# Kernel optimization log

Hardware: AMD Instinct MI355X
Metric: run time of the kernel (lower is better)

Reference implementation:

```python
import jax, jax.numpy as jnp
import numpy as np

N_CLASS, EMB, NH = 32000, 128, 256
B, T = 2048, 256


def setup_inputs() -> dict:
    key = jax.random.key(0)
    ks = iter(jax.random.split(key, 40))
    d = {}
    d["X"] = jax.random.randint(next(ks), (B, T), 0, N_CLASS)
    d["C"] = jax.random.normal(next(ks), (N_CLASS, EMB), jnp.float32) * 0.02
    for g in "ifco":
        d[f"U_{g}1"] = jax.random.normal(next(ks), (EMB, NH), jnp.float32) / np.sqrt(EMB)
        d[f"V_{g}1"] = jax.random.normal(next(ks), (NH, NH), jnp.float32) / np.sqrt(NH)
        d[f"U_{g}2"] = jax.random.normal(next(ks), (NH, NH), jnp.float32) / np.sqrt(NH)
        d[f"V_{g}2"] = jax.random.normal(next(ks), (NH, NH), jnp.float32) / np.sqrt(NH)
        d[f"b_{g}1"] = jnp.ones((NH,), jnp.float32)
    d["W_out"] = jax.random.normal(next(ks), (NH, N_CLASS), jnp.float32) / np.sqrt(NH)
    d["b_out"] = jnp.ones((N_CLASS,), jnp.float32)
    return d


def reference(X, C,
              U_i1, V_i1, U_i2, V_i2, b_i1,
              U_f1, V_f1, U_f2, V_f2, b_f1,
              U_c1, V_c1, U_c2, V_c2, b_c1,
              U_o1, V_o1, U_o2, V_o2, b_o1,
              W_out, b_out):
    # Embed then move time to the leading axis: [T, B, EMB]
    xs = jnp.transpose(C[X], (1, 0, 2))
    Bsz = X.shape[0]
    dtype = C.dtype
    z = jnp.zeros((Bsz, NH), dtype)

    def step(carry, x):
        h1, c1, h2, c2 = carry
        # layer 1 LSTM cell
        f1 = jax.nn.sigmoid(x @ U_f1 + h1 @ V_f1 + b_f1)
        i1 = jax.nn.sigmoid(x @ U_i1 + h1 @ V_i1 + b_i1)
        g1 = jnp.tanh(x @ U_c1 + h1 @ V_c1 + b_c1)
        c1n = c1 * f1 + i1 * g1
        o1 = jax.nn.sigmoid(x @ U_o1 + h1 @ V_o1 + b_o1)
        h1n = o1 * jnp.tanh(c1n)
        # layer 2 LSTM cell (NOTE: original code reuses layer-1 biases here)
        f2 = jax.nn.sigmoid(h1n @ U_f2 + h2 @ V_f2 + b_f1)
        i2 = jax.nn.sigmoid(h1n @ U_i2 + h2 @ V_i2 + b_i1)
        g2 = jnp.tanh(h1n @ U_c2 + h2 @ V_c2 + b_c1)
        c2n = c2 * f2 + i2 * g2
        o2 = jax.nn.sigmoid(h1n @ U_o2 + h2 @ V_o2 + b_o1)
        h2n = o2 * jnp.tanh(c2n)
        return (h1n, c1n, h2n, c2n), None

    (h1, c1, h2, c2), _ = jax.lax.scan(step, (z, z, z, z), xs)
    return h2 @ W_out + b_out  # [B, N_CLASS]
```

## Files before the change

### kernel.cpp

```cpp
#include <hip/hip_runtime.h>
#include <hip/hip_bf16.h>

#define B_SZ   2048
#define T_SZ   256
#define EMB    128
#define NH     256
#define NCLASS 32000

typedef __bf16 bf16;
typedef __bf16 bf16x8 __attribute__((ext_vector_type(8)));
typedef __bf16 bf16x4 __attribute__((ext_vector_type(4)));
typedef float  f32x4  __attribute__((ext_vector_type(4)));

__device__ __forceinline__ float sigf(float x)      { return 1.0f / (1.0f + __expf(-x)); }
__device__ __forceinline__ float tanhfast(float x)  { return 2.0f / (1.0f + __expf(-2.0f * x)) - 1.0f; }

struct GatePtrs {
    const float* U1[4];
    const float* V1[4];
    const float* U2[4];
    const float* V2[4];
};

__global__ void prep_w1(GatePtrs gp, bf16* __restrict__ Wt1) {
    int gc = blockIdx.x;
    int k  = threadIdx.x;
    int g  = (gc >> 4) & 3;
    int nh = ((gc >> 6) << 4) | (gc & 15);
    float v = (k < EMB) ? gp.U1[g][k * NH + nh] : gp.V1[g][(k - EMB) * NH + nh];
    Wt1[gc * 384 + k] = (bf16)v;
}

__global__ void prep_w2(GatePtrs gp, bf16* __restrict__ Wt2) {
    int gc = blockIdx.x;
    int k  = threadIdx.x;
    int g  = (gc >> 4) & 3;
    int nh = ((gc >> 6) << 4) | (gc & 15);
    float v = (k < NH) ? gp.U2[g][k * NH + nh] : gp.V2[g][(k - NH) * NH + nh];
    Wt2[gc * 512 + k] = (bf16)v;
}

__global__ void prep_wo(const float* __restrict__ Wo, bf16* __restrict__ WoT) {
    __shared__ float tile[32][33];
    int n0 = blockIdx.x * 32;
    int k0 = blockIdx.y * 32;
    int tx = threadIdx.x & 31;
    int ty = threadIdx.x >> 5;
#pragma unroll
    for (int i = 0; i < 4; i++) {
        int k = k0 + ty + i * 8;
        tile[ty + i * 8][tx] = Wo[(size_t)k * NCLASS + n0 + tx];
    }
    __syncthreads();
#pragma unroll
    for (int i = 0; i < 4; i++) {
        int n = n0 + ty + i * 8;
        WoT[(size_t)n * NH + k0 + tx] = (bf16)tile[tx][ty + i * 8];
    }
}

__global__ void prep_xe(const int* __restrict__ X, const float* __restrict__ C,
                        bf16* __restrict__ Xe) {
    size_t id = (size_t)blockIdx.x * 256 + threadIdx.x;
    int c4 = (int)(id & 31) * 4;
    int b  = (int)(id >> 5) & (B_SZ - 1);
    int t  = (int)(id >> 16);
    int idx = X[b * T_SZ + t];
    float4 v = *(const float4*)(C + (size_t)idx * EMB + c4);
    bf16x4 hv;
    hv[0] = (bf16)v.x; hv[1] = (bf16)v.y; hv[2] = (bf16)v.z; hv[3] = (bf16)v.w;
    *(bf16x4*)(Xe + ((size_t)t * B_SZ + b) * EMB + c4) = hv;
}

template<int PRE>
__global__ __launch_bounds__(1024, 1) void lstm_kernel(
    const int* __restrict__ X, const float* __restrict__ C,
    const bf16* __restrict__ Wt1, const bf16* __restrict__ Wt2,
    const float* __restrict__ bi, const float* __restrict__ bf_,
    const float* __restrict__ bc, const float* __restrict__ bo,
    const bf16* __restrict__ Xe,
    bf16* __restrict__ h2out)
{
    __shared__ bf16 A1[2][32][392];
    __shared__ bf16 A2[2][32][520];

    const int tid  = threadIdx.x;
    const int lane = tid & 63;
    const int wv   = tid >> 6;
    const int cl   = lane & 15;
    const int quad = lane >> 4;
    const int gb   = blockIdx.x * 32;

    const float* bp[4] = { bi, bf_, bc, bo };
    float bias[4];
#pragma unroll
    for (int g = 0; g < 4; g++) bias[g] = bp[g][wv * 16 + cl];

    const bf16* w1p[4];
    const bf16* w2p[4];
#pragma unroll
    for (int g = 0; g < 4; g++) {
        int gc = wv * 64 + g * 16 + cl;
        w1p[g] = Wt1 + gc * 384 + quad * 8;
        w2p[g] = Wt2 + gc * 512 + quad * 8;
    }

    for (int i = tid; i < 8192; i += 1024) {
        int r = i >> 8, c = i & 255;
        A1[0][r][128 + c] = (bf16)0.0f;
        A2[0][r][256 + c] = (bf16)0.0f;
    }
    {
        int r  = tid >> 5;
        int cc = (tid & 31) * 4;
        if (PRE) {
            bf16x4 hv = *(const bf16x4*)(Xe + ((size_t)0 * B_SZ + gb + r) * EMB + cc);
            *(bf16x4*)&A1[0][r][cc] = hv;
        } else {
            int idx = X[(gb + r) * T_SZ + 0];
            float4 v = *(const float4*)(C + (size_t)idx * EMB + cc);
            bf16x4 hv;
            hv[0] = (bf16)v.x; hv[1] = (bf16)v.y; hv[2] = (bf16)v.z; hv[3] = (bf16)v.w;
            *(bf16x4*)&A1[0][r][cc] = hv;
        }
    }

    f32x4 c1s[2], c2s[2];
    const f32x4 zf = { 0.0f, 0.0f, 0.0f, 0.0f };
#pragma unroll
    for (int mt = 0; mt < 2; mt++) { c1s[mt] = zf; c2s[mt] = zf; }

    __syncthreads();

    for (int t = 0; t < T_SZ; t++) {
        const int p = t & 1;

        f32x4 acc[2][4];
#pragma unroll
        for (int mt = 0; mt < 2; mt++)
#pragma unroll
            for (int g = 0; g < 4; g++) acc[mt][g] = zf;

        {
            const bf16* a0p = &A1[p][cl][quad * 8];
            const bf16* a1p = &A1[p][16 + cl][quad * 8];
#pragma unroll
            for (int kt = 0; kt < 12; kt++) {
                bf16x8 a0 = *(const bf16x8*)(a0p + kt * 32);
                bf16x8 a1 = *(const bf16x8*)(a1p + kt * 32);
#pragma unroll
                for (int g = 0; g < 4; g++) {
                    bf16x8 b = *(const bf16x8*)(w1p[g] + kt * 32);
                    acc[0][g] = __builtin_amdgcn_mfma_f32_16x16x32_bf16(a0, b, acc[0][g], 0, 0, 0);
                    acc[1][g] = __builtin_amdgcn_mfma_f32_16x16x32_bf16(a1, b, acc[1][g], 0, 0, 0);
                }
            }
        }

#pragma unroll
        for (int mt = 0; mt < 2; mt++)
#pragma unroll
            for (int r = 0; r < 4; r++) {
                float iv = sigf(acc[mt][0][r] + bias[0]);
                float fv = sigf(acc[mt][1][r] + bias[1]);
                float gv = tanhfast(acc[mt][2][r] + bias[2]);
                float ov = sigf(acc[mt][3][r] + bias[3]);
                float c  = c1s[mt][r] * fv + iv * gv;
                c1s[mt][r] = c;
                float h  = ov * tanhfast(c);
                int row = mt * 16 + quad * 4 + r;
                int col = wv * 16 + cl;
                bf16 hb = (bf16)h;
                A1[p ^ 1][row][128 + col] = hb;
                A2[p][row][col]           = hb;
            }

        if (t + 1 < T_SZ) {
            int r  = tid >> 5;
            int cc = (tid & 31) * 4;
            if (PRE) {
                bf16x4 hv = *(const bf16x4*)(Xe + ((size_t)(t + 1) * B_SZ + gb + r) * EMB + cc);
                *(bf16x4*)&A1[p ^ 1][r][cc] = hv;
            } else {
                int idx = X[(gb + r) * T_SZ + (t + 1)];
                float4 v = *(const float4*)(C + (size_t)idx * EMB + cc);
                bf16x4 hv;
                hv[0] = (bf16)v.x; hv[1] = (bf16)v.y; hv[2] = (bf16)v.z; hv[3] = (bf16)v.w;
                *(bf16x4*)&A1[p ^ 1][r][cc] = hv;
            }
        }

        __syncthreads();

#pragma unroll
        for (int mt = 0; mt < 2; mt++)
#pragma unroll
            for (int g = 0; g < 4; g++) acc[mt][g] = zf;

        {
            const bf16* a0p = &A2[p][cl][quad * 8];
            const bf16* a1p = &A2[p][16 + cl][quad * 8];
#pragma unroll
            for (int kt = 0; kt < 16; kt++) {
                bf16x8 a0 = *(const bf16x8*)(a0p + kt * 32);
                bf16x8 a1 = *(const bf16x8*)(a1p + kt * 32);
#pragma unroll
                for (int g = 0; g < 4; g++) {
                    bf16x8 b = *(const bf16x8*)(w2p[g] + kt * 32);
                    acc[0][g] = __builtin_amdgcn_mfma_f32_16x16x32_bf16(a0, b, acc[0][g], 0, 0, 0);
                    acc[1][g] = __builtin_amdgcn_mfma_f32_16x16x32_bf16(a1, b, acc[1][g], 0, 0, 0);
                }
            }
        }

#pragma unroll
        for (int mt = 0; mt < 2; mt++)
#pragma unroll
            for (int r = 0; r < 4; r++) {
                float iv = sigf(acc[mt][0][r] + bias[0]);
                float fv = sigf(acc[mt][1][r] + bias[1]);
                float gv = tanhfast(acc[mt][2][r] + bias[2]);
                float ov = sigf(acc[mt][3][r] + bias[3]);
                float c  = c2s[mt][r] * fv + iv * gv;
                c2s[mt][r] = c;
                float h  = ov * tanhfast(c);
                int row = mt * 16 + quad * 4 + r;
                int col = wv * 16 + cl;
                A2[p ^ 1][row][256 + col] = (bf16)h;
            }
    }

    __syncthreads();
    for (int i = tid; i < 8192; i += 1024) {
        int r = i >> 8, c = i & 255;
        h2out[(size_t)(gb + r) * NH + c] = A2[0][r][256 + c];
    }
}

__global__ __launch_bounds__(256, 1) void out_gemm(
    const bf16* __restrict__ h2, const bf16* __restrict__ WoT,
    const float* __restrict__ bout, float* __restrict__ out)
{
    const int tid  = threadIdx.x;
    const int lane = tid & 63;
    const int wv   = tid >> 6;
    const int cl   = lane & 15;
    const int quad = lane >> 4;
    const int nb   = blockIdx.x;
    const int mb   = blockIdx.y;
    const int mbase = mb * 64 + wv * 16;
    const int nbase = nb * 64;

    f32x4 acc[4];
    const f32x4 zf = { 0.0f, 0.0f, 0.0f, 0.0f };
#pragma unroll
    for (int nt = 0; nt < 4; nt++) acc[nt] = zf;

#pragma unroll
    for (int kt = 0; kt < 8; kt++) {
        bf16x8 a = *(const bf16x8*)(h2 + (size_t)(mbase + cl) * NH + kt * 32 + quad * 8);
#pragma unroll
        for (int nt = 0; nt < 4; nt++) {
            bf16x8 b = *(const bf16x8*)(WoT + (size_t)(nbase + nt * 16 + cl) * NH + kt * 32 + quad * 8);
            acc[nt] = __builtin_amdgcn_mfma_f32_16x16x32_bf16(a, b, acc[nt], 0, 0, 0);
        }
    }
#pragma unroll
    for (int nt = 0; nt < 4; nt++) {
        int col = nbase + nt * 16 + cl;
        float bv = bout[col];
#pragma unroll
        for (int r = 0; r < 4; r++) {
            int row = mbase + quad * 4 + r;
            out[(size_t)row * NCLASS + col] = acc[nt][r] + bv;
        }
    }
}

extern "C" void kernel_launch(void* const* d_in, const int* in_sizes, int n_in,
                              void* d_out, int out_size, void* d_ws, size_t ws_size,
                              hipStream_t stream) {
    const int*   X  = (const int*)d_in[0];
    const float* C  = (const float*)d_in[1];
    GatePtrs gp;
    for (int g = 0; g < 4; g++) {
        int base = 2 + 5 * g;
        gp.U1[g] = (const float*)d_in[base + 0];
        gp.V1[g] = (const float*)d_in[base + 1];
        gp.U2[g] = (const float*)d_in[base + 2];
        gp.V2[g] = (const float*)d_in[base + 3];
    }
    const float* bi   = (const float*)d_in[6];
    const float* bf_  = (const float*)d_in[11];
    const float* bc   = (const float*)d_in[16];
    const float* bo   = (const float*)d_in[21];
    const float* Wo   = (const float*)d_in[22];
    const float* bout = (const float*)d_in[23];
    float* out = (float*)d_out;

    char* ws = (char*)d_ws;
    bf16* Wt1 = (bf16*)(ws);
    bf16* Wt2 = (bf16*)(ws + 786432);
    bf16* WoT = (bf16*)(ws + 786432 + 1048576);
    bf16* h2w = (bf16*)(ws + 786432 + 1048576 + 16384000);
    bf16* Xe  = (bf16*)(ws + 786432 + 1048576 + 16384000 + 1048576);
    const size_t WS_NEED_XE = 786432ull + 1048576 + 16384000 + 1048576 + 134217728;

    prep_w1<<<dim3(1024), dim3(384), 0, stream>>>(gp, Wt1);
    prep_w2<<<dim3(1024), dim3(512), 0, stream>>>(gp, Wt2);
    prep_wo<<<dim3(1000, 8), dim3(256), 0, stream>>>(Wo, WoT);

    if (ws_size >= WS_NEED_XE) {
        prep_xe<<<dim3(65536), dim3(256), 0, stream>>>(X, C, Xe);
        lstm_kernel<1><<<dim3(64), dim3(1024), 0, stream>>>(X, C, Wt1, Wt2, bi, bf_, bc, bo, Xe, h2w);
    } else {
        lstm_kernel<0><<<dim3(64), dim3(1024), 0, stream>>>(X, C, Wt1, Wt2, bi, bf_, bc, bo, Xe, h2w);
    }

    out_gemm<<<dim3(500, 32), dim3(256), 0, stream>>>(h2w, WoT, bout, out);
}
```

Before: 13.06 ms.

## Software-pipeline weight fragment loads through a rotating register buffer across both layers

Weight fragments are now prefetched into a three-slot register ring: each MFMA k-step consumes one slot while loading the fragment needed three steps later. The ring wraps from layer-1 weights into layer-2 weights and back, so loads for the next phase begin before the current phase ends. The next timestep's embedding row is also loaded at the top of the step, which hides its global latency behind the layer-1 GEMM. The launch bound's minimum block count is raised from 1 to 4. That lowers the per-thread register budget while the ring adds roughly 48 live registers, so spilling is a real risk, and the LDS footprint of about 116 KB still allows only one block per CU.

```diff
diff --git a/kernel.cpp b/kernel.cpp
--- a/kernel.cpp
+++ b/kernel.cpp
@@ -73,7 +73,7 @@
 }
 
 template<int PRE>
-__global__ __launch_bounds__(1024, 1) void lstm_kernel(
+__global__ __launch_bounds__(1024, 4) void lstm_kernel(
     const int* __restrict__ X, const float* __restrict__ C,
     const bf16* __restrict__ Wt1, const bf16* __restrict__ Wt2,
     const float* __restrict__ bi, const float* __restrict__ bf_,
@@ -96,14 +96,20 @@
 #pragma unroll
     for (int g = 0; g < 4; g++) bias[g] = bp[g][wv * 16 + cl];
 
-    const bf16* w1p[4];
-    const bf16* w2p[4];
+    int o1[4], o2[4];
 #pragma unroll
     for (int g = 0; g < 4; g++) {
         int gc = wv * 64 + g * 16 + cl;
-        w1p[g] = Wt1 + gc * 384 + quad * 8;
-        w2p[g] = Wt2 + gc * 512 + quad * 8;
-    }
+        o1[g] = gc * 384 + quad * 8;
+        o2[g] = gc * 512 + quad * 8;
+    }
+
+    bf16x8 bb[3][4];
+#pragma unroll
+    for (int s = 0; s < 3; s++)
+#pragma unroll
+        for (int g = 0; g < 4; g++)
+            bb[s][g] = *(const bf16x8*)(Wt1 + o1[g] + s * 32);
 
     for (int i = tid; i < 8192; i += 1024) {
         int r = i >> 8, c = i & 255;
@@ -135,6 +141,20 @@
     for (int t = 0; t < T_SZ; t++) {
         const int p = t & 1;
 
+        bf16x4 xv;
+        {
+            int r  = tid >> 5;
+            int cc = (tid & 31) * 4;
+            int tn = (t + 1 < T_SZ) ? (t + 1) : t;
+            if (PRE) {
+                xv = *(const bf16x4*)(Xe + ((size_t)tn * B_SZ + gb + r) * EMB + cc);
+            } else {
+                int idx = X[(gb + r) * T_SZ + tn];
+                float4 v = *(const float4*)(C + (size_t)idx * EMB + cc);
+                xv[0] = (bf16)v.x; xv[1] = (bf16)v.y; xv[2] = (bf16)v.z; xv[3] = (bf16)v.w;
+            }
+        }
+
         f32x4 acc[2][4];
 #pragma unroll
         for (int mt = 0; mt < 2; mt++)
@@ -148,11 +168,16 @@
             for (int kt = 0; kt < 12; kt++) {
                 bf16x8 a0 = *(const bf16x8*)(a0p + kt * 32);
                 bf16x8 a1 = *(const bf16x8*)(a1p + kt * 32);
+                const int s = kt % 3;
 #pragma unroll
                 for (int g = 0; g < 4; g++) {
-                    bf16x8 b = *(const bf16x8*)(w1p[g] + kt * 32);
-                    acc[0][g] = __builtin_amdgcn_mfma_f32_16x16x32_bf16(a0, b, acc[0][g], 0, 0, 0);
-                    acc[1][g] = __builtin_amdgcn_mfma_f32_16x16x32_bf16(a1, b, acc[1][g], 0, 0, 0);
+                    acc[0][g] = __builtin_amdgcn_mfma_f32_16x16x32_bf16(a0, bb[s][g], acc[0][g], 0, 0, 0);
+                    acc[1][g] = __builtin_amdgcn_mfma_f32_16x16x32_bf16(a1, bb[s][g], acc[1][g], 0, 0, 0);
+                }
+#pragma unroll
+                for (int g = 0; g < 4; g++) {
+                    if (kt < 9) bb[s][g] = *(const bf16x8*)(Wt1 + o1[g] + (kt + 3) * 32);
+                    else        bb[s][g] = *(const bf16x8*)(Wt2 + o2[g] + s * 32);
                 }
             }
         }
@@ -175,19 +200,10 @@
                 A2[p][row][col]           = hb;
             }
 
-        if (t + 1 < T_SZ) {
+        {
             int r  = tid >> 5;
             int cc = (tid & 31) * 4;
-            if (PRE) {
-                bf16x4 hv = *(const bf16x4*)(Xe + ((size_t)(t + 1) * B_SZ + gb + r) * EMB + cc);
-                *(bf16x4*)&A1[p ^ 1][r][cc] = hv;
-            } else {
-                int idx = X[(gb + r) * T_SZ + (t + 1)];
-                float4 v = *(const float4*)(C + (size_t)idx * EMB + cc);
-                bf16x4 hv;
-                hv[0] = (bf16)v.x; hv[1] = (bf16)v.y; hv[2] = (bf16)v.z; hv[3] = (bf16)v.w;
-                *(bf16x4*)&A1[p ^ 1][r][cc] = hv;
-            }
+            *(bf16x4*)&A1[p ^ 1][r][cc] = xv;
         }
 
         __syncthreads();
@@ -204,11 +220,16 @@
             for (int kt = 0; kt < 16; kt++) {
                 bf16x8 a0 = *(const bf16x8*)(a0p + kt * 32);
                 bf16x8 a1 = *(const bf16x8*)(a1p + kt * 32);
+                const int s = kt % 3;
 #pragma unroll
                 for (int g = 0; g < 4; g++) {
-                    bf16x8 b = *(const bf16x8*)(w2p[g] + kt * 32);
-                    acc[0][g] = __builtin_amdgcn_mfma_f32_16x16x32_bf16(a0, b, acc[0][g], 0, 0, 0);
-                    acc[1][g] = __builtin_amdgcn_mfma_f32_16x16x32_bf16(a1, b, acc[1][g], 0, 0, 0);
+                    acc[0][g] = __builtin_amdgcn_mfma_f32_16x16x32_bf16(a0, bb[s][g], acc[0][g], 0, 0, 0);
+                    acc[1][g] = __builtin_amdgcn_mfma_f32_16x16x32_bf16(a1, bb[s][g], acc[1][g], 0, 0, 0);
+                }
+#pragma unroll
+                for (int g = 0; g < 4; g++) {
+                    if (kt < 13) bb[s][g] = *(const bf16x8*)(Wt2 + o2[g] + (kt + 3) * 32);
+                    else         bb[s][g] = *(const bf16x8*)(Wt1 + o1[g] + s * 32);
                 }
             }
         }
```

Result: slower. 13.72 ms (+5.0%).

## Halve LSTM batch tile per block to 16 rows and double-buffer weight loads

Applied to the files above, without the earlier changes.

Each LSTM block now handles 16 batch rows instead of 32, so the grid doubles from 64 to 128 blocks and more of the machine's compute units take part in the serial recurrence. Weight fragments are loaded one k-step ahead into a register double buffer, with a scheduling barrier placed before each group of MFMAs. The load for the next layer's first k-step is issued during the last step of the current layer. The cost is that each weight fragment fetched from global/L2 memory now feeds half as many MFMAs, roughly doubling total weight traffic per timestep, and launch_bounds is changed to allow 4 blocks per CU.

```diff
diff --git a/kernel.cpp b/kernel.cpp
--- a/kernel.cpp
+++ b/kernel.cpp
@@ -10,6 +10,7 @@
 typedef __bf16 bf16;
 typedef __bf16 bf16x8 __attribute__((ext_vector_type(8)));
 typedef __bf16 bf16x4 __attribute__((ext_vector_type(4)));
+typedef __bf16 bf16x2 __attribute__((ext_vector_type(2)));
 typedef float  f32x4  __attribute__((ext_vector_type(4)));
 
 __device__ __forceinline__ float sigf(float x)      { return 1.0f / (1.0f + __expf(-x)); }
@@ -73,7 +74,7 @@
 }
 
 template<int PRE>
-__global__ __launch_bounds__(1024, 1) void lstm_kernel(
+__global__ __launch_bounds__(1024, 4) void lstm_kernel(
     const int* __restrict__ X, const float* __restrict__ C,
     const bf16* __restrict__ Wt1, const bf16* __restrict__ Wt2,
     const float* __restrict__ bi, const float* __restrict__ bf_,
@@ -81,157 +82,154 @@
     const bf16* __restrict__ Xe,
     bf16* __restrict__ h2out)
 {
-    __shared__ bf16 A1[2][32][392];
-    __shared__ bf16 A2[2][32][520];
+    __shared__ bf16 A1[2][16][392];
+    __shared__ bf16 A2[2][16][520];
 
     const int tid  = threadIdx.x;
     const int lane = tid & 63;
     const int wv   = tid >> 6;
     const int cl   = lane & 15;
     const int quad = lane >> 4;
-    const int gb   = blockIdx.x * 32;
+    const int gb   = blockIdx.x * 16;
 
     const float* bp[4] = { bi, bf_, bc, bo };
     float bias[4];
 #pragma unroll
     for (int g = 0; g < 4; g++) bias[g] = bp[g][wv * 16 + cl];
 
-    const bf16* w1p[4];
-    const bf16* w2p[4];
+    const bf16* w1b[4];
+    const bf16* w2b[4];
 #pragma unroll
     for (int g = 0; g < 4; g++) {
-        int gc = wv * 64 + g * 16 + cl;
-        w1p[g] = Wt1 + gc * 384 + quad * 8;
-        w2p[g] = Wt2 + gc * 512 + quad * 8;
-    }
-
-    for (int i = tid; i < 8192; i += 1024) {
+        w1b[g] = Wt1 + g * (16 * 384);
+        w2b[g] = Wt2 + g * (16 * 512);
+    }
+    const int o1 = (wv * 64 + cl) * 384 + quad * 8;
+    const int o2 = (wv * 64 + cl) * 512 + quad * 8;
+
+    bf16x8 bb[2][4];
+#pragma unroll
+    for (int g = 0; g < 4; g++)
+        bb[0][g] = *(const bf16x8*)(w1b[g] + o1);
+
+    for (int i = tid; i < 4096; i += 1024) {
         int r = i >> 8, c = i & 255;
         A1[0][r][128 + c] = (bf16)0.0f;
         A2[0][r][256 + c] = (bf16)0.0f;
     }
     {
-        int r  = tid >> 5;
-        int cc = (tid & 31) * 4;
+        int r  = tid >> 6;
+        int cc = (tid & 63) * 2;
         if (PRE) {
-            bf16x4 hv = *(const bf16x4*)(Xe + ((size_t)0 * B_SZ + gb + r) * EMB + cc);
-            *(bf16x4*)&A1[0][r][cc] = hv;
+            bf16x2 hv = *(const bf16x2*)(Xe + ((size_t)0 * B_SZ + gb + r) * EMB + cc);
+            *(bf16x2*)&A1[0][r][cc] = hv;
         } else {
             int idx = X[(gb + r) * T_SZ + 0];
-            float4 v = *(const float4*)(C + (size_t)idx * EMB + cc);
-            bf16x4 hv;
-            hv[0] = (bf16)v.x; hv[1] = (bf16)v.y; hv[2] = (bf16)v.z; hv[3] = (bf16)v.w;
-            *(bf16x4*)&A1[0][r][cc] = hv;
-        }
-    }
-
-    f32x4 c1s[2], c2s[2];
+            float2 v = *(const float2*)(C + (size_t)idx * EMB + cc);
+            bf16x2 hv; hv[0] = (bf16)v.x; hv[1] = (bf16)v.y;
+            *(bf16x2*)&A1[0][r][cc] = hv;
+        }
+    }
+
+    f32x4 c1s, c2s;
     const f32x4 zf = { 0.0f, 0.0f, 0.0f, 0.0f };
-#pragma unroll
-    for (int mt = 0; mt < 2; mt++) { c1s[mt] = zf; c2s[mt] = zf; }
+    c1s = zf; c2s = zf;
 
     __syncthreads();
 
     for (int t = 0; t < T_SZ; t++) {
         const int p = t & 1;
 
-        f32x4 acc[2][4];
-#pragma unroll
-        for (int mt = 0; mt < 2; mt++)
-#pragma unroll
-            for (int g = 0; g < 4; g++) acc[mt][g] = zf;
+        f32x4 acc[4];
+#pragma unroll
+        for (int g = 0; g < 4; g++) acc[g] = zf;
 
         {
             const bf16* a0p = &A1[p][cl][quad * 8];
-            const bf16* a1p = &A1[p][16 + cl][quad * 8];
 #pragma unroll
             for (int kt = 0; kt < 12; kt++) {
                 bf16x8 a0 = *(const bf16x8*)(a0p + kt * 32);
-                bf16x8 a1 = *(const bf16x8*)(a1p + kt * 32);
 #pragma unroll
                 for (int g = 0; g < 4; g++) {
-                    bf16x8 b = *(const bf16x8*)(w1p[g] + kt * 32);
-                    acc[0][g] = __builtin_amdgcn_mfma_f32_16x16x32_bf16(a0, b, acc[0][g], 0, 0, 0);
-                    acc[1][g] = __builtin_amdgcn_mfma_f32_16x16x32_bf16(a1, b, acc[1][g], 0, 0, 0);
+                    if (kt < 11) bb[(kt + 1) & 1][g] = *(const bf16x8*)(w1b[g] + o1 + (kt + 1) * 32);
+                    else         bb[0][g]            = *(const bf16x8*)(w2b[g] + o2);
                 }
+                __builtin_amdgcn_sched_barrier(0);
+#pragma unroll
+                for (int g = 0; g < 4; g++)
+                    acc[g] = __builtin_amdgcn_mfma_f32_16x16x32_bf16(a0, bb[kt & 1][g], acc[g], 0, 0, 0);
             }
         }
 
 #pragma unroll
-        for (int mt = 0; mt < 2; mt++)
-#pragma unroll
-            for (int r = 0; r < 4; r++) {
-                float iv = sigf(acc[mt][0][r] + bias[0]);
-                float fv = sigf(acc[mt][1][r] + bias[1]);
-                float gv = tanhfast(acc[mt][2][r] + bias[2]);
-                float ov = sigf(acc[mt][3][r] + bias[3]);
-                float c  = c1s[mt][r] * fv + iv * gv;
-                c1s[mt][r] = c;
-                float h  = ov * tanhfast(c);
-                int row = mt * 16 + quad * 4 + r;
-                int col = wv * 16 + cl;
-                bf16 hb = (bf16)h;
-                A1[p ^ 1][row][128 + col] = hb;
-                A2[p][row][col]           = hb;
-            }
+        for (int r = 0; r < 4; r++) {
+            float iv = sigf(acc[0][r] + bias[0]);
+            float fv = sigf(acc[1][r] + bias[1]);
+            float gv = tanhfast(acc[2][r] + bias[2]);
+            float ov = sigf(acc[3][r] + bias[3]);
+            float c  = c1s[r] * fv + iv * gv;
+            c1s[r] = c;
+            float h  = ov * tanhfast(c);
+            int row = quad * 4 + r;
+            int col = wv * 16 + cl;
+            bf16 hb = (bf16)h;
+            A1[p ^ 1][row][128 + col] = hb;
+            A2[p][row][col]           = hb;
+        }
 
         if (t + 1 < T_SZ) {
-            int r  = tid >> 5;
-            int cc = (tid & 31) * 4;
+            int r  = tid >> 6;
+            int cc = (tid & 63) * 2;
             if (PRE) {
-                bf16x4 hv = *(const bf16x4*)(Xe + ((size_t)(t + 1) * B_SZ + gb + r) * EMB + cc);
-                *(bf16x4*)&A1[p ^ 1][r][cc] = hv;
+                bf16x2 hv = *(const bf16x2*)(Xe + ((size_t)(t + 1) * B_SZ + gb + r) * EMB + cc);
+                *(bf16x2*)&A1[p ^ 1][r][cc] = hv;
             } else {
                 int idx = X[(gb + r) * T_SZ + (t + 1)];
-                float4 v = *(const float4*)(C + (size_t)idx * EMB + cc);
-                bf16x4 hv;
-                hv[0] = (bf16)v.x; hv[1] = (bf16)v.y; hv[2] = (bf16)v.z; hv[3] = (bf16)v.w;
-                *(bf16x4*)&A1[p ^ 1][r][cc] = hv;
+                float2 v = *(const float2*)(C + (size_t)idx * EMB + cc);
+                bf16x2 hv; hv[0] = (bf16)v.x; hv[1] = (bf16)v.y;
+                *(bf16x2*)&A1[p ^ 1][r][cc] = hv;
             }
         }
 
         __syncthreads();
 
 #pragma unroll
-        for (int mt = 0; mt < 2; mt++)
-#pragma unroll
-            for (int g = 0; g < 4; g++) acc[mt][g] = zf;
+        for (int g = 0; g < 4; g++) acc[g] = zf;
 
         {
             const bf16* a0p = &A2[p][cl][quad * 8];
-            const bf16* a1p = &A2[p][16 + cl][quad * 8];
 #pragma unroll
             for (int kt = 0; kt < 16; kt++) {
                 bf16x8 a0 = *(const bf16x8*)(a0p + kt * 32);
-                bf16x8 a1 = *(const bf16x8*)(a1p + kt * 32);
 #pragma unroll
                 for (int g = 0; g < 4; g++) {
-                    bf16x8 b = *(const bf16x8*)(w2p[g] + kt * 32);
-                    acc[0][g] = __builtin_amdgcn_mfma_f32_16x16x32_bf16(a0, b, acc[0][g], 0, 0, 0);
-                    acc[1][g] = __builtin_amdgcn_mfma_f32_16x16x32_bf16(a1, b, acc[1][g], 0, 0, 0);
+                    if (kt < 15) bb[(kt + 1) & 1][g] = *(const bf16x8*)(w2b[g] + o2 + (kt + 1) * 32);
+                    else         bb[0][g]            = *(const bf16x8*)(w1b[g] + o1);
                 }
+                __builtin_amdgcn_sched_barrier(0);
+#pragma unroll
+                for (int g = 0; g < 4; g++)
+                    acc[g] = __builtin_amdgcn_mfma_f32_16x16x32_bf16(a0, bb[kt & 1][g], acc[g], 0, 0, 0);
             }
         }
 
 #pragma unroll
-        for (int mt = 0; mt < 2; mt++)
-#pragma unroll
-            for (int r = 0; r < 4; r++) {
-                float iv = sigf(acc[mt][0][r] + bias[0]);
-                float fv = sigf(acc[mt][1][r] + bias[1]);
-                float gv = tanhfast(acc[mt][2][r] + bias[2]);
-                float ov = sigf(acc[mt][3][r] + bias[3]);
-                float c  = c2s[mt][r] * fv + iv * gv;
-                c2s[mt][r] = c;
-                float h  = ov * tanhfast(c);
-                int row = mt * 16 + quad * 4 + r;
-                int col = wv * 16 + cl;
-                A2[p ^ 1][row][256 + col] = (bf16)h;
-            }
+        for (int r = 0; r < 4; r++) {
+            float iv = sigf(acc[0][r] + bias[0]);
+            float fv = sigf(acc[1][r] + bias[1]);
+            float gv = tanhfast(acc[2][r] + bias[2]);
+            float ov = sigf(acc[3][r] + bias[3]);
+            float c  = c2s[r] * fv + iv * gv;
+            c2s[r] = c;
+            float h  = ov * tanhfast(c);
+            int row = quad * 4 + r;
+            int col = wv * 16 + cl;
+            A2[p ^ 1][row][256 + col] = (bf16)h;
+        }
     }
 
     __syncthreads();
-    for (int i = tid; i < 8192; i += 1024) {
+    for (int i = tid; i < 4096; i += 1024) {
         int r = i >> 8, c = i & 255;
         h2out[(size_t)(gb + r) * NH + c] = A2[0][r][256 + c];
     }
@@ -312,9 +310,9 @@
 
     if (ws_size >= WS_NEED_XE) {
         prep_xe<<<dim3(65536), dim3(256), 0, stream>>>(X, C, Xe);
-        lstm_kernel<1><<<dim3(64), dim3(1024), 0, stream>>>(X, C, Wt1, Wt2, bi, bf_, bc, bo, Xe, h2w);
+        lstm_kernel<1><<<dim3(128), dim3(1024), 0, stream>>>(X, C, Wt1, Wt2, bi, bf_, bc, bo, Xe, h2w);
     } else {
-        lstm_kernel<0><<<dim3(64), dim3(1024), 0, stream>>>(X, C, Wt1, Wt2, bi, bf_, bc, bo, Xe, h2w);
+        lstm_kernel<0><<<dim3(128), dim3(1024), 0, stream>>>(X, C, Wt1, Wt2, bi, bf_, bc, bo, Xe, h2w);
     }
 
     out_gemm<<<dim3(500, 32), dim3(256), 0, stream>>>(h2w, WoT, bout, out);
```

After: 14.63 ms. 12.0% more time.
